# Performance work log

Hardware: AMD Instinct MI355X
Metric: run time of the kernel (lower is better)

## Reference

```python
import jax, jax.numpy as jnp
import numpy as np

B, F, C, NS, P, N = 256, 2048, 16384, 65536, 8, 32
T, W_BU, W_H, P_MARGIN, N_MARGIN = 1.0, 1.0, 10.0, 0.1, 0.1


def setup_inputs() -> dict:
    key = jax.random.key(0)
    ks = jax.random.split(key, 8)
    inputs = jax.random.normal(ks[0], (B, F), jnp.float32)
    targets = jax.random.randint(ks[1], (B,), 0, C)
    # batch global indices: unique (original .item() assumes a single match)
    indexs = jax.random.permutation(ks[2], NS)[:B].astype(jnp.int64) if False else jax.random.permutation(ks[2], jnp.arange(NS))[:B]
    # positive candidates drawn from in-batch indices so they are found in `indexs`
    pos_sel = jax.random.randint(ks[3], (B, P), 0, B)
    ppairs = indexs[pos_sel]
    # negative candidates: arbitrary global indices (mostly not in batch)
    npairs = jax.random.randint(ks[4], (B, N), 0, NS)
    all_label_to_clusterid = jax.random.randint(ks[5], (NS,), 0, C)
    V = jax.random.normal(ks[6], (C, F), jnp.float32)
    V = V / jnp.linalg.norm(V, axis=1, keepdims=True)  # bank rows are L2-normalized by the update rule
    return {"inputs": inputs, "targets": targets, "ppairs": ppairs, "npairs": npairs,
            "indexs": indexs, "all_label_to_clusterid": all_label_to_clusterid, "V": V, "epoch": 1}


def _forward(inputs, targets, ppairs, npairs, indexs, all_label_to_clusterid, V, epoch):
    # Exclusive branch: logits against the memory bank (V treated as constant)
    outputs = (inputs @ V.T) * T  # [B, C]
    logp = jax.nn.log_softmax(outputs, axis=1)
    bu_loss = -jnp.mean(jnp.take_along_axis(logp, targets[:, None], axis=1))

    # ms_loss (use_prior=True, use_table=True)
    ni = inputs / jnp.linalg.norm(inputs, axis=1, keepdims=True)
    sims = ni @ ni.T          # [B, B]
    tsims = ni @ V.T          # [B, C]

    # positives found in the batch: (ppair == indexs).nonzero()
    mp = ppairs[:, :, None] == indexs[None, None, :]        # [B, P, B]
    found_p = jnp.any(mp, axis=2)
    idx_p = jnp.argmax(mp, axis=2)
    psim_b = jnp.take_along_axis(sims, idx_p, axis=1)       # [B, P]
    mask_pb = found_p & (ppairs >= 0)
    # table positive: tsims[i, target] appended if nonzero
    tp = jnp.take_along_axis(tsims, targets[:, None], axis=1)  # [B, 1]
    mask_tp = tp != 0
    psims = jnp.concatenate([psim_b, tp], axis=1)           # [B, P+1]
    pmask = jnp.concatenate([mask_pb, mask_tp], axis=1)

    # negatives found in the batch
    mn = npairs[:, :, None] == indexs[None, None, :]        # [B, N, B]
    found_n = jnp.any(mn, axis=2)
    idx_n = jnp.argmax(mn, axis=2)
    nsim_b = jnp.take_along_axis(sims, idx_n, axis=1)       # [B, N]
    mask_nb = found_n & (npairs >= 0)
    # table negative appended for EVERY npair (indent level in original): tsims[i, clusterid[npair]]
    ncid = all_label_to_clusterid[jnp.clip(npairs, 0, None)]
    tn = jnp.take_along_axis(tsims, ncid, axis=1)           # [B, N]
    mask_tn = (npairs >= 0) & (tn != 0)
    nsims = jnp.concatenate([nsim_b, tn], axis=1)           # [B, 2N]
    nmask = jnp.concatenate([mask_nb, mask_tn], axis=1)

    # thresholds: max(nsims) or -3 (+p_margin); min(psims) or 3 (-n_margin)
    p_thrd = jnp.where(jnp.any(nmask, 1), jnp.max(jnp.where(nmask, nsims, -jnp.inf), 1), -3.0) + P_MARGIN
    n_thrd = jnp.where(jnp.any(pmask, 1), jnp.min(jnp.where(pmask, psims, jnp.inf), 1), 3.0) - N_MARGIN

    hp = pmask & (psims < p_thrd[:, None])
    hn = nmask & (nsims > n_thrd[:, None]) & (nsims < 0.999999)

    hp_sum = jnp.sum(jnp.where(hp, jnp.exp(-2.0 * (psims - 0.5)), 0.0))
    hn_sum = jnp.sum(jnp.where(hn, jnp.exp(50.0 * (nsims - 0.5)), 0.0))
    hp_loss = jnp.where(jnp.any(hp), 0.5 * jnp.log1p(hp_sum), 0.0)
    hn_loss = jnp.where(jnp.any(hn), (1.0 / 50.0) * jnp.log1p(hn_sum), 0.0)
    # original builds hpsims/hnsims with torch.tensor(...), which DETACHES them
    h_loss = jax.lax.stop_gradient(hp_loss + hn_loss)

    loss = W_BU * bu_loss + W_H * h_loss
    return loss, outputs


def reference(inputs, targets, ppairs, npairs, indexs, all_label_to_clusterid, V, epoch):
    return _forward(inputs, targets, ppairs, npairs, indexs, all_label_to_clusterid, V, epoch)
```

## Files before the change

kernel.cpp:

```cpp
#include <hip/hip_runtime.h>
#include <hip/hip_bf16.h>
#include <math.h>

#define B_SZ 256
#define F_SZ 2048
#define C_SZ 16384
#define P_SZ 8
#define N_SZ 32
#define NTILE 128

typedef __bf16 bf16x8 __attribute__((ext_vector_type(8)));
typedef float f32x4 __attribute__((ext_vector_type(4)));
typedef unsigned short us8 __attribute__((ext_vector_type(8)));

typedef __attribute__((address_space(3))) unsigned int lds_u32;
typedef __attribute__((address_space(1))) const unsigned int glb_u32;

#define WAITCNT_VM6   0x0F76
#define WAITCNT_VM0   0x0F70

__device__ __forceinline__ unsigned short f2bf(float x) {
    union { float f; unsigned int u; } v; v.f = x;
    unsigned int r = v.u + 0x7FFFu + ((v.u >> 16) & 1u);
    return (unsigned short)(r >> 16);
}

__device__ __forceinline__ unsigned int pk2bf(float x, float y) {
    union { float f; unsigned int u; } a, b; a.f = x; b.f = y;
    return __builtin_amdgcn_perm(b.u + 0x8000u, a.u + 0x8000u, 0x07060302u);
}

__global__ __launch_bounds__(256) void prep_kernel(const float* __restrict__ inputs,
                                                   unsigned short* __restrict__ Abf,
                                                   float* __restrict__ norms) {
    const int row = blockIdx.x;
    const int tid = threadIdx.x;
    const float* rp = inputs + (size_t)row * F_SZ + tid * 8;
    float4 v0 = *(const float4*)(rp);
    float4 v1 = *(const float4*)(rp + 4);
    us8 o;
    o[0]=f2bf(v0.x); o[1]=f2bf(v0.y); o[2]=f2bf(v0.z); o[3]=f2bf(v0.w);
    o[4]=f2bf(v1.x); o[5]=f2bf(v1.y); o[6]=f2bf(v1.z); o[7]=f2bf(v1.w);
    *(us8*)(Abf + (size_t)row * F_SZ + tid * 8) = o;
    float ss = v0.x*v0.x + v0.y*v0.y + v0.z*v0.z + v0.w*v0.w
             + v1.x*v1.x + v1.y*v1.y + v1.z*v1.z + v1.w*v1.w;
    __shared__ float red[256];
    red[tid] = ss; __syncthreads();
    for (int s = 128; s > 0; s >>= 1) { if (tid < s) red[tid] += red[tid+s]; __syncthreads(); }
    if (tid == 0) norms[row] = sqrtf(red[0]);
}

#define BM 128
#define BN 128
#define BK 64
#define KITERS (F_SZ / BK)

__global__ __launch_bounds__(512, 1) void gemm_kernel(const unsigned short* __restrict__ Abf,
                                                      const float* __restrict__ V,
                                                      float* __restrict__ Cout,
                                                      float* __restrict__ pmax,
                                                      float* __restrict__ psum) {
    __shared__ unsigned short As[3][BM * BK];
    __shared__ float Bs[3][BN * BK];
    __shared__ float sm[BM * 4], ss2[BM * 4];

    const int tid = threadIdx.x;
    const int lane = tid & 63;
    const int w = tid >> 6;
    const int wm = w & 1, wn = w >> 1;
    const int q = lane >> 4, l16 = lane & 15;

    const int bid = blockIdx.x;
    const int mhalf = (bid >> 3) & 1;
    const int slab  = (bid & 7) | ((bid >> 4) << 3);
    const int bm0 = mhalf * BM;
    const int bn0 = slab * BN;

    f32x4 acc[4][2];
    #pragma unroll
    for (int i = 0; i < 4; i++)
        #pragma unroll
        for (int j = 0; j < 2; j++) acc[i][j] = (f32x4){0.f, 0.f, 0.f, 0.f};

    int aS0 = w * 128 + lane;
    int aS1 = aS0 + 64;
    const int ar0 = aS0 >> 3, ag0 = (aS0 & 7) ^ (ar0 & 7);
    const int ar1 = aS1 >> 3, ag1 = (aS1 & 7) ^ (ar1 & 7);
    const unsigned short* Ag0 = Abf + (size_t)(bm0 + ar0) * F_SZ + ag0 * 8;
    const unsigned short* Ag1 = Abf + (size_t)(bm0 + ar1) * F_SZ + ag1 * 8;

    int bS[4]; const float* Bg[4];
    #pragma unroll
    for (int j = 0; j < 4; ++j) {
        bS[j] = w * 256 + j * 64 + lane;
        const int col = bS[j] >> 4, gc = (bS[j] & 15) ^ (col & 15);
        Bg[j] = V + (size_t)(bn0 + col) * F_SZ + gc * 4;
    }
    const int aDst0 = (w * 128) * 8, aDst1 = (w * 128 + 64) * 8;

    auto issue = [&](int ring, int k0) {
        __builtin_amdgcn_global_load_lds((glb_u32*)(Ag0 + k0), (lds_u32*)&As[ring][aDst0], 16, 0, 0);
        __builtin_amdgcn_global_load_lds((glb_u32*)(Ag1 + k0), (lds_u32*)&As[ring][aDst1], 16, 0, 0);
        #pragma unroll
        for (int j = 0; j < 4; ++j)
            __builtin_amdgcn_global_load_lds((glb_u32*)(Bg[j] + k0), (lds_u32*)&Bs[ring][(w * 256 + j * 64) * 4], 16, 0, 0);
    };
    auto compute = [&](int ring) {
        #pragma unroll
        for (int ks = 0; ks < 2; ++ks) {
            bf16x8 af[4], bfv[2];
            const int kc = ks * 4 + q;
            #pragma unroll
            for (int mi = 0; mi < 4; ++mi) {
                const int row = wm * 64 + mi * 16 + l16;
                af[mi] = *(const bf16x8*)&As[ring][row * 64 + ((kc ^ (row & 7)) * 8)];
            }
            #pragma unroll
            for (int ni = 0; ni < 2; ++ni) {
                const int col = wn * 32 + ni * 16 + l16;
                const int c0 = ks * 8 + q * 2;
                float4 f0 = *(const float4*)&Bs[ring][col * 64 + ((c0 ^ (col & 15)) * 4)];
                float4 f1 = *(const float4*)&Bs[ring][col * 64 + (((c0 + 1) ^ (col & 15)) * 4)];
                union { uint4 u; bf16x8 b; } cv;
                cv.u = (uint4){ pk2bf(f0.x, f0.y), pk2bf(f0.z, f0.w),
                                pk2bf(f1.x, f1.y), pk2bf(f1.z, f1.w) };
                bfv[ni] = cv.b;
            }
            #pragma unroll
            for (int mi = 0; mi < 4; ++mi)
                #pragma unroll
                for (int ni = 0; ni < 2; ++ni)
                    acc[mi][ni] = __builtin_amdgcn_mfma_f32_16x16x32_bf16(af[mi], bfv[ni], acc[mi][ni], 0, 0, 0);
        }
    };

    issue(0, 0);
    issue(1, BK);
    __builtin_amdgcn_s_waitcnt(WAITCNT_VM6);
    __builtin_amdgcn_s_barrier();

    int cur = 0;
    #pragma unroll 1
    for (int it = 0; it < KITERS; ++it) {
        const int nxt2 = (cur == 0) ? 2 : cur - 1;
        if (it + 2 < KITERS) issue(nxt2, (it + 2) * BK);
        compute(cur);
        if (it + 2 < KITERS)      __builtin_amdgcn_s_waitcnt(WAITCNT_VM6);
        else if (it + 1 < KITERS) __builtin_amdgcn_s_waitcnt(WAITCNT_VM0);
        if (it + 1 < KITERS) __builtin_amdgcn_s_barrier();
        cur = (cur == 2) ? 0 : cur + 1;
    }

    #pragma unroll
    for (int mi = 0; mi < 4; ++mi) {
        const int r0 = bm0 + wm * 64 + mi * 16 + q * 4;
        #pragma unroll
        for (int ni = 0; ni < 2; ++ni) {
            const int c0g = bn0 + wn * 32 + ni * 16 + l16;
            #pragma unroll
            for (int r = 0; r < 4; ++r)
                Cout[(size_t)(r0 + r) * C_SZ + c0g] = acc[mi][ni][r];
        }
    }

    #pragma unroll
    for (int mi = 0; mi < 4; ++mi) {
        #pragma unroll
        for (int r = 0; r < 4; ++r) {
            float mloc = fmaxf(acc[mi][0][r], acc[mi][1][r]);
            #pragma unroll
            for (int off = 1; off < 16; off <<= 1)
                mloc = fmaxf(mloc, __shfl_xor(mloc, off, 64));
            float sloc = __expf(acc[mi][0][r] - mloc) + __expf(acc[mi][1][r] - mloc);
            #pragma unroll
            for (int off = 1; off < 16; off <<= 1)
                sloc += __shfl_xor(sloc, off, 64);
            if (l16 == 0) {
                const int lrow = wm * 64 + mi * 16 + q * 4 + r;
                sm[lrow * 4 + wn] = mloc;
                ss2[lrow * 4 + wn] = sloc;
            }
        }
    }
    __syncthreads();
    if (tid < BM) {
        float m = -INFINITY, s = 0.f;
        #pragma unroll
        for (int v = 0; v < 4; ++v) {
            float m2 = sm[tid * 4 + v], s2 = ss2[tid * 4 + v];
            float nm = fmaxf(m, m2);
            s = s * __expf(m - nm) + s2 * __expf(m2 - nm);
            m = nm;
        }
        pmax[(bm0 + tid) * NTILE + slab] = m;
        psum[(bm0 + tid) * NTILE + slab] = s;
    }
}

__global__ __launch_bounds__(256) void pairs_kernel(
    const float* __restrict__ inputs, const int* __restrict__ targets,
    const int* __restrict__ ppairs, const int* __restrict__ npairs,
    const int* __restrict__ indexs, const int* __restrict__ cluster,
    const float* __restrict__ outputs, const float* __restrict__ norms,
    const float* __restrict__ pmax, const float* __restrict__ psum,
    float* __restrict__ bu_part, float* __restrict__ hp_part,
    float* __restrict__ hn_part, int* __restrict__ flag_part)
{
    const int i = blockIdx.x;
    const int tid = threadIdx.x;
    __shared__ int idxbuf[B_SZ];
    __shared__ int pj[P_SZ];
    __shared__ int nj[N_SZ];
    __shared__ float simp[P_SZ];
    __shared__ float simn[N_SZ];
    __shared__ float tnv[N_SZ];
    __shared__ float s_tp;
    __shared__ float rm[NTILE], rs[NTILE];

    idxbuf[tid] = indexs[tid];
    if (tid < NTILE) {
        rm[tid] = pmax[i * NTILE + tid];
        rs[tid] = psum[i * NTILE + tid];
    }
    __syncthreads();
    for (int s = NTILE / 2; s > 0; s >>= 1) {
        if (tid < s) {
            float a = rm[tid], sa = rs[tid];
            float b = rm[tid + s], sb = rs[tid + s];
            float nn = fmaxf(a, b);
            rs[tid] = sa * __expf(a - nn) + sb * __expf(b - nn);
            rm[tid] = nn;
        }
        __syncthreads();
    }

    const float* row = outputs + (size_t)i * C_SZ;
    const float ni_norm = norms[i];

    if (tid == 0) {
        float logZ = rm[0] + logf(rs[0]);
        bu_part[i] = -(row[targets[i]] - logZ);
    }

    if (tid < P_SZ) {
        int pp = ppairs[i * P_SZ + tid];
        int f = -1;
        if (pp >= 0) for (int j = 0; j < B_SZ; j++) if (idxbuf[j] == pp) { f = j; break; }
        pj[tid] = f;
    } else if (tid < P_SZ + N_SZ) {
        int t = tid - P_SZ;
        int np = npairs[i * N_SZ + t];
        int f = -1;
        if (np >= 0) for (int j = 0; j < B_SZ; j++) if (idxbuf[j] == np) { f = j; break; }
        nj[t] = f;
        int cid = cluster[np < 0 ? 0 : np];
        tnv[t] = row[cid] / ni_norm;
    }
    if (tid == P_SZ + N_SZ) s_tp = row[targets[i]] / ni_norm;
    __syncthreads();

    const int lane = tid & 63, wv = tid >> 6;
    for (int qq = wv; qq < P_SZ + N_SZ; qq += 4) {
        int j = (qq < P_SZ) ? pj[qq] : nj[qq - P_SZ];
        float s = 0.f;
        if (j >= 0) {
            const float* xi = inputs + (size_t)i * F_SZ;
            const float* xj = inputs + (size_t)j * F_SZ;
            float d = 0.f;
            for (int k = lane; k < F_SZ; k += 64) d += xi[k] * xj[k];
            for (int off = 32; off > 0; off >>= 1) d += __shfl_down(d, off);
            s = d / (ni_norm * norms[j]);
        }
        if (lane == 0) { if (qq < P_SZ) simp[qq] = s; else simn[qq - P_SZ] = s; }
    }
    __syncthreads();

    if (tid == 0) {
        float psims[P_SZ + 1]; bool pmask[P_SZ + 1];
        for (int p = 0; p < P_SZ; p++) {
            int pp = ppairs[i * P_SZ + p];
            pmask[p] = (pj[p] >= 0) && (pp >= 0);
            psims[p] = simp[p];
        }
        psims[P_SZ] = s_tp; pmask[P_SZ] = (s_tp != 0.0f);

        float nsims[2 * N_SZ]; bool nmask[2 * N_SZ];
        for (int t = 0; t < N_SZ; t++) {
            int np = npairs[i * N_SZ + t];
            nmask[t] = (nj[t] >= 0) && (np >= 0);
            nsims[t] = simn[t];
            nsims[N_SZ + t] = tnv[t];
            nmask[N_SZ + t] = (np >= 0) && (tnv[t] != 0.0f);
        }
        bool anyp = false, anyn = false;
        float maxn = -INFINITY, minp = INFINITY;
        for (int t = 0; t < 2 * N_SZ; t++) if (nmask[t]) { anyn = true; maxn = fmaxf(maxn, nsims[t]); }
        for (int p = 0; p < P_SZ + 1; p++) if (pmask[p]) { anyp = true; minp = fminf(minp, psims[p]); }
        float p_thrd = (anyn ? maxn : -3.0f) + 0.1f;
        float n_thrd = (anyp ? minp : 3.0f) - 0.1f;
        float hps = 0.f, hns = 0.f; int fl = 0;
        for (int p = 0; p < P_SZ + 1; p++)
            if (pmask[p] && psims[p] < p_thrd) { fl |= 1; hps += expf(-2.0f * (psims[p] - 0.5f)); }
        for (int t = 0; t < 2 * N_SZ; t++)
            if (nmask[t] && nsims[t] > n_thrd && nsims[t] < 0.999999f) { fl |= 2; hns += expf(50.0f * (nsims[t] - 0.5f)); }
        hp_part[i] = hps; hn_part[i] = hns; flag_part[i] = fl;
    }
}

__global__ __launch_bounds__(256) void finalize_kernel(
    const float* __restrict__ bu_part, const float* __restrict__ hp_part,
    const float* __restrict__ hn_part, const int* __restrict__ flag_part,
    float* __restrict__ d_out)
{
    __shared__ float r1[256], r2[256], r3[256];
    __shared__ int rf[256];
    const int tid = threadIdx.x;
    r1[tid] = bu_part[tid]; r2[tid] = hp_part[tid]; r3[tid] = hn_part[tid]; rf[tid] = flag_part[tid];
    __syncthreads();
    for (int s = 128; s > 0; s >>= 1) {
        if (tid < s) { r1[tid] += r1[tid+s]; r2[tid] += r2[tid+s]; r3[tid] += r3[tid+s]; rf[tid] |= rf[tid+s]; }
        __syncthreads();
    }
    if (tid == 0) {
        float bu = r1[0] / (float)B_SZ;
        float hp_loss = (rf[0] & 1) ? 0.5f * log1pf(r2[0]) : 0.0f;
        float hn_loss = (rf[0] & 2) ? (1.0f / 50.0f) * log1pf(r3[0]) : 0.0f;
        d_out[0] = 1.0f * bu + 10.0f * (hp_loss + hn_loss);
    }
}

extern "C" void kernel_launch(void* const* d_in, const int* in_sizes, int n_in,
                              void* d_out, int out_size, void* d_ws, size_t ws_size,
                              hipStream_t stream) {
    const float* inputs  = (const float*)d_in[0];
    const int*   targets = (const int*)d_in[1];
    const int*   ppairs  = (const int*)d_in[2];
    const int*   npairs  = (const int*)d_in[3];
    const int*   indexs  = (const int*)d_in[4];
    const int*   cluster = (const int*)d_in[5];
    const float* V       = (const float*)d_in[6];
    float* out = (float*)d_out;

    char* ws = (char*)d_ws;
    unsigned short* Abf = (unsigned short*)ws;
    float* norms   = (float*)(ws + (size_t)B_SZ * F_SZ * 2);
    float* bu_part = norms + B_SZ;
    float* hp_part = bu_part + B_SZ;
    float* hn_part = hp_part + B_SZ;
    int*   flag_part = (int*)(hn_part + B_SZ);
    float* pmax = (float*)(flag_part + B_SZ);
    float* psum = pmax + (size_t)B_SZ * NTILE;

    prep_kernel<<<B_SZ, 256, 0, stream>>>(inputs, Abf, norms);
    gemm_kernel<<<256, 512, 0, stream>>>(Abf, V, out + 1, pmax, psum);
    pairs_kernel<<<B_SZ, 256, 0, stream>>>(inputs, targets, ppairs, npairs, indexs,
                                           cluster, out + 1, norms, pmax, psum,
                                           bu_part, hp_part, hn_part, flag_part);
    finalize_kernel<<<1, 256, 0, stream>>>(bu_part, hp_part, hn_part, flag_part, out);
}
```

Baseline: 308.0 us.

## Pre-convert V to bf16 in a separate kernel and retile the GEMM

Adds a kernel that converts the fp32 memory bank V to bf16 in workspace before the GEMM. The GEMM then loads bf16 tiles for both operands directly into LDS, so the per-iteration fp32-to-bf16 packing inside the main loop goes away. The GEMM is also restructured: 256 threads with 64x64 warp tiles, a 128-wide K phase, and a double buffer in place of the triple ring with explicit waitcnt. The trade-off is an extra full pass over V, which reads 128MB and writes 64MB, plus a 64MB larger workspace footprint. The plain __syncthreads after each phase also allows less load/compute overlap than the old scheme.

After: 329.9 us. 7.1% more time.

```diff
diff --git a/kernel.cpp b/kernel.cpp
--- a/kernel.cpp
+++ b/kernel.cpp
@@ -16,18 +16,10 @@
 typedef __attribute__((address_space(3))) unsigned int lds_u32;
 typedef __attribute__((address_space(1))) const unsigned int glb_u32;
 
-#define WAITCNT_VM6   0x0F76
-#define WAITCNT_VM0   0x0F70
-
 __device__ __forceinline__ unsigned short f2bf(float x) {
     union { float f; unsigned int u; } v; v.f = x;
     unsigned int r = v.u + 0x7FFFu + ((v.u >> 16) & 1u);
     return (unsigned short)(r >> 16);
-}
-
-__device__ __forceinline__ unsigned int pk2bf(float x, float y) {
-    union { float f; unsigned int u; } a, b; a.f = x; b.f = y;
-    return __builtin_amdgcn_perm(b.u + 0x8000u, a.u + 0x8000u, 0x07060302u);
 }
 
 __global__ __launch_bounds__(256) void prep_kernel(const float* __restrict__ inputs,
@@ -50,24 +42,35 @@
     if (tid == 0) norms[row] = sqrtf(red[0]);
 }
 
+__global__ __launch_bounds__(256) void vcvt_kernel(const float* __restrict__ V,
+                                                   unsigned short* __restrict__ Vbf) {
+    const size_t idx = ((size_t)blockIdx.x * 256 + threadIdx.x) * 8;
+    float4 a = *(const float4*)(V + idx);
+    float4 b = *(const float4*)(V + idx + 4);
+    us8 o;
+    o[0]=f2bf(a.x); o[1]=f2bf(a.y); o[2]=f2bf(a.z); o[3]=f2bf(a.w);
+    o[4]=f2bf(b.x); o[5]=f2bf(b.y); o[6]=f2bf(b.z); o[7]=f2bf(b.w);
+    *(us8*)(Vbf + idx) = o;
+}
+
 #define BM 128
 #define BN 128
-#define BK 64
-#define KITERS (F_SZ / BK)
-
-__global__ __launch_bounds__(512, 1) void gemm_kernel(const unsigned short* __restrict__ Abf,
-                                                      const float* __restrict__ V,
+#define PH 128
+#define NPHASE (F_SZ / PH)
+
+__global__ __launch_bounds__(256, 1) void gemm_kernel(const unsigned short* __restrict__ Abf,
+                                                      const unsigned short* __restrict__ Vbf,
                                                       float* __restrict__ Cout,
                                                       float* __restrict__ pmax,
                                                       float* __restrict__ psum) {
-    __shared__ unsigned short As[3][BM * BK];
-    __shared__ float Bs[3][BN * BK];
-    __shared__ float sm[BM * 4], ss2[BM * 4];
+    __shared__ unsigned short As[2][BM * PH];
+    __shared__ unsigned short Bs[2][BN * PH];
+    __shared__ float sm[BM * 2], ss2[BM * 2];
 
     const int tid = threadIdx.x;
     const int lane = tid & 63;
     const int w = tid >> 6;
-    const int wm = w & 1, wn = w >> 1;
+    const int wm = w >> 1, wn = w & 1;
     const int q = lane >> 4, l16 = lane & 15;
 
     const int bid = blockIdx.x;
@@ -76,87 +79,73 @@
     const int bm0 = mhalf * BM;
     const int bn0 = slab * BN;
 
-    f32x4 acc[4][2];
+    f32x4 acc[4][4];
     #pragma unroll
     for (int i = 0; i < 4; i++)
         #pragma unroll
-        for (int j = 0; j < 2; j++) acc[i][j] = (f32x4){0.f, 0.f, 0.f, 0.f};
-
-    int aS0 = w * 128 + lane;
-    int aS1 = aS0 + 64;
-    const int ar0 = aS0 >> 3, ag0 = (aS0 & 7) ^ (ar0 & 7);
-    const int ar1 = aS1 >> 3, ag1 = (aS1 & 7) ^ (ar1 & 7);
-    const unsigned short* Ag0 = Abf + (size_t)(bm0 + ar0) * F_SZ + ag0 * 8;
-    const unsigned short* Ag1 = Abf + (size_t)(bm0 + ar1) * F_SZ + ag1 * 8;
-
-    int bS[4]; const float* Bg[4];
-    #pragma unroll
-    for (int j = 0; j < 4; ++j) {
-        bS[j] = w * 256 + j * 64 + lane;
-        const int col = bS[j] >> 4, gc = (bS[j] & 15) ^ (col & 15);
-        Bg[j] = V + (size_t)(bn0 + col) * F_SZ + gc * 4;
-    }
-    const int aDst0 = (w * 128) * 8, aDst1 = (w * 128 + 64) * 8;
-
-    auto issue = [&](int ring, int k0) {
-        __builtin_amdgcn_global_load_lds((glb_u32*)(Ag0 + k0), (lds_u32*)&As[ring][aDst0], 16, 0, 0);
-        __builtin_amdgcn_global_load_lds((glb_u32*)(Ag1 + k0), (lds_u32*)&As[ring][aDst1], 16, 0, 0);
-        #pragma unroll
-        for (int j = 0; j < 4; ++j)
-            __builtin_amdgcn_global_load_lds((glb_u32*)(Bg[j] + k0), (lds_u32*)&Bs[ring][(w * 256 + j * 64) * 4], 16, 0, 0);
+        for (int j = 0; j < 4; j++) acc[i][j] = (f32x4){0.f, 0.f, 0.f, 0.f};
+
+    const int sr = tid >> 4;
+    const int scl = tid & 15;
+    const int gkc = (scl & 8) | ((scl & 7) ^ (sr & 7));
+    const unsigned short* Abase = Abf + (size_t)(bm0 + sr) * F_SZ + gkc * 8;
+    const unsigned short* Bbase = Vbf + (size_t)(bn0 + sr) * F_SZ + gkc * 8;
+
+    auto issueAB = [&](int buf, int p) {
+        const int ko = p * PH;
+        #pragma unroll
+        for (int i = 0; i < 8; ++i)
+            __builtin_amdgcn_global_load_lds(
+                (glb_u32*)(Abase + (size_t)i * 16 * F_SZ + ko),
+                (lds_u32*)&As[buf][(i * 256 + tid) * 8], 16, 0, 0);
+        #pragma unroll
+        for (int i = 0; i < 8; ++i)
+            __builtin_amdgcn_global_load_lds(
+                (glb_u32*)(Bbase + (size_t)i * 16 * F_SZ + ko),
+                (lds_u32*)&Bs[buf][(i * 256 + tid) * 8], 16, 0, 0);
     };
-    auto compute = [&](int ring) {
-        #pragma unroll
-        for (int ks = 0; ks < 2; ++ks) {
-            bf16x8 af[4], bfv[2];
-            const int kc = ks * 4 + q;
+    auto compute = [&](int buf) {
+        #pragma unroll
+        for (int s = 0; s < 4; ++s) {
+            const int kc = s * 4 + q;
+            bf16x8 af[4], bf[4];
             #pragma unroll
             for (int mi = 0; mi < 4; ++mi) {
                 const int row = wm * 64 + mi * 16 + l16;
-                af[mi] = *(const bf16x8*)&As[ring][row * 64 + ((kc ^ (row & 7)) * 8)];
+                const int sc = (kc & 8) | ((kc & 7) ^ (row & 7));
+                af[mi] = *(const bf16x8*)&As[buf][(row * 16 + sc) * 8];
             }
             #pragma unroll
-            for (int ni = 0; ni < 2; ++ni) {
-                const int col = wn * 32 + ni * 16 + l16;
-                const int c0 = ks * 8 + q * 2;
-                float4 f0 = *(const float4*)&Bs[ring][col * 64 + ((c0 ^ (col & 15)) * 4)];
-                float4 f1 = *(const float4*)&Bs[ring][col * 64 + (((c0 + 1) ^ (col & 15)) * 4)];
-                union { uint4 u; bf16x8 b; } cv;
-                cv.u = (uint4){ pk2bf(f0.x, f0.y), pk2bf(f0.z, f0.w),
-                                pk2bf(f1.x, f1.y), pk2bf(f1.z, f1.w) };
-                bfv[ni] = cv.b;
+            for (int ni = 0; ni < 4; ++ni) {
+                const int col = wn * 64 + ni * 16 + l16;
+                const int sc = (kc & 8) | ((kc & 7) ^ (col & 7));
+                bf[ni] = *(const bf16x8*)&Bs[buf][(col * 16 + sc) * 8];
             }
             #pragma unroll
             for (int mi = 0; mi < 4; ++mi)
                 #pragma unroll
-                for (int ni = 0; ni < 2; ++ni)
-                    acc[mi][ni] = __builtin_amdgcn_mfma_f32_16x16x32_bf16(af[mi], bfv[ni], acc[mi][ni], 0, 0, 0);
+                for (int ni = 0; ni < 4; ++ni)
+                    acc[mi][ni] = __builtin_amdgcn_mfma_f32_16x16x32_bf16(af[mi], bf[ni], acc[mi][ni], 0, 0, 0);
         }
     };
 
-    issue(0, 0);
-    issue(1, BK);
-    __builtin_amdgcn_s_waitcnt(WAITCNT_VM6);
-    __builtin_amdgcn_s_barrier();
-
-    int cur = 0;
+    issueAB(0, 0);
+    __syncthreads();
+
     #pragma unroll 1
-    for (int it = 0; it < KITERS; ++it) {
-        const int nxt2 = (cur == 0) ? 2 : cur - 1;
-        if (it + 2 < KITERS) issue(nxt2, (it + 2) * BK);
-        compute(cur);
-        if (it + 2 < KITERS)      __builtin_amdgcn_s_waitcnt(WAITCNT_VM6);
-        else if (it + 1 < KITERS) __builtin_amdgcn_s_waitcnt(WAITCNT_VM0);
-        if (it + 1 < KITERS) __builtin_amdgcn_s_barrier();
-        cur = (cur == 2) ? 0 : cur + 1;
+    for (int p = 0; p < NPHASE; ++p) {
+        const int buf = p & 1;
+        if (p + 1 < NPHASE) issueAB(buf ^ 1, p + 1);
+        compute(buf);
+        __syncthreads();
     }
 
     #pragma unroll
     for (int mi = 0; mi < 4; ++mi) {
         const int r0 = bm0 + wm * 64 + mi * 16 + q * 4;
         #pragma unroll
-        for (int ni = 0; ni < 2; ++ni) {
-            const int c0g = bn0 + wn * 32 + ni * 16 + l16;
+        for (int ni = 0; ni < 4; ++ni) {
+            const int c0g = bn0 + wn * 64 + ni * 16 + l16;
             #pragma unroll
             for (int r = 0; r < 4; ++r)
                 Cout[(size_t)(r0 + r) * C_SZ + c0g] = acc[mi][ni][r];
@@ -167,32 +156,30 @@
     for (int mi = 0; mi < 4; ++mi) {
         #pragma unroll
         for (int r = 0; r < 4; ++r) {
-            float mloc = fmaxf(acc[mi][0][r], acc[mi][1][r]);
+            float mloc = fmaxf(fmaxf(acc[mi][0][r], acc[mi][1][r]),
+                               fmaxf(acc[mi][2][r], acc[mi][3][r]));
             #pragma unroll
             for (int off = 1; off < 16; off <<= 1)
                 mloc = fmaxf(mloc, __shfl_xor(mloc, off, 64));
-            float sloc = __expf(acc[mi][0][r] - mloc) + __expf(acc[mi][1][r] - mloc);
+            float sloc = __expf(acc[mi][0][r] - mloc) + __expf(acc[mi][1][r] - mloc)
+                       + __expf(acc[mi][2][r] - mloc) + __expf(acc[mi][3][r] - mloc);
             #pragma unroll
             for (int off = 1; off < 16; off <<= 1)
                 sloc += __shfl_xor(sloc, off, 64);
             if (l16 == 0) {
                 const int lrow = wm * 64 + mi * 16 + q * 4 + r;
-                sm[lrow * 4 + wn] = mloc;
-                ss2[lrow * 4 + wn] = sloc;
+                sm[lrow * 2 + wn] = mloc;
+                ss2[lrow * 2 + wn] = sloc;
             }
         }
     }
     __syncthreads();
     if (tid < BM) {
-        float m = -INFINITY, s = 0.f;
-        #pragma unroll
-        for (int v = 0; v < 4; ++v) {
-            float m2 = sm[tid * 4 + v], s2 = ss2[tid * 4 + v];
-            float nm = fmaxf(m, m2);
-            s = s * __expf(m - nm) + s2 * __expf(m2 - nm);
-            m = nm;
-        }
-        pmax[(bm0 + tid) * NTILE + slab] = m;
+        float m1 = sm[tid * 2], s1 = ss2[tid * 2];
+        float m2 = sm[tid * 2 + 1], s2 = ss2[tid * 2 + 1];
+        float nm = fmaxf(m1, m2);
+        float s = s1 * __expf(m1 - nm) + s2 * __expf(m2 - nm);
+        pmax[(bm0 + tid) * NTILE + slab] = nm;
         psum[(bm0 + tid) * NTILE + slab] = s;
     }
 }
@@ -343,7 +330,8 @@
 
     char* ws = (char*)d_ws;
     unsigned short* Abf = (unsigned short*)ws;
-    float* norms   = (float*)(ws + (size_t)B_SZ * F_SZ * 2);
+    unsigned short* Vbf = (unsigned short*)(ws + (size_t)B_SZ * F_SZ * 2);
+    float* norms   = (float*)(ws + (size_t)B_SZ * F_SZ * 2 + (size_t)C_SZ * F_SZ * 2);
     float* bu_part = norms + B_SZ;
     float* hp_part = bu_part + B_SZ;
     float* hn_part = hp_part + B_SZ;
@@ -352,7 +340,8 @@
     float* psum = pmax + (size_t)B_SZ * NTILE;
 
     prep_kernel<<<B_SZ, 256, 0, stream>>>(inputs, Abf, norms);
-    gemm_kernel<<<256, 512, 0, stream>>>(Abf, V, out + 1, pmax, psum);
+    vcvt_kernel<<<(C_SZ * F_SZ) / (256 * 8), 256, 0, stream>>>(V, Vbf);
+    gemm_kernel<<<256, 256, 0, stream>>>(Abf, Vbf, out + 1, pmax, psum);
     pairs_kernel<<<B_SZ, 256, 0, stream>>>(inputs, targets, ppairs, npairs, indexs,
                                            cluster, out + 1, norms, pmax, psum,
                                            bu_part, hp_part, hn_part, flag_part);
```
